# Optimization experiments

Hardware: AMD Instinct MI355X
Metric: run time of the kernel (lower is better)

## Reference

```python
import jax, jax.numpy as jnp
import numpy as np


def setup_inputs() -> dict:
    key = jax.random.key(0)
    k1, k2, k3 = jax.random.split(key, 3)
    H, W, C = 200, 200, 512
    NUM_ROIS = 300
    img = jax.random.normal(k1, (1, H, W, C), dtype=jnp.float32)
    # rois[0, r] = (x, y, w, h); ensure crops are in-bounds and non-empty
    xy = jax.random.randint(k2, (1, NUM_ROIS, 2), 0, 100)
    wh = jax.random.randint(k3, (1, NUM_ROIS, 2), 1, 100)
    rois = jnp.concatenate([xy, wh], axis=-1).astype(jnp.int32)
    return {"img": img, "rois": rois, "pool_size": 7}


def reference(img, rois, pool_size):
    """RoiPoolingConv: per-ROI crop + legacy-TF bilinear resize, vectorized.

    img:  [1, H, W, C] float feature map
    rois: [1, R, 4] int (x, y, w, h) in feature-map pixels
    returns [1, R, P, P, C]
    """
    P = pool_size
    img0 = img[0]                              # [H, W, C]
    H, W, C = img0.shape
    x = rois[0, :, 0].astype(jnp.int32)        # [R]
    y = rois[0, :, 1].astype(jnp.int32)
    w = rois[0, :, 2].astype(jnp.int32)
    h = rois[0, :, 3].astype(jnp.int32)

    out_idx = jnp.arange(P, dtype=jnp.float32)  # [P]
    # legacy tf.image.resize_images (bilinear, align_corners=False):
    #   src = out_idx * (in_size / out_size); corners floor(src), floor(src)+1 clipped
    sy = y[:, None].astype(jnp.float32) + out_idx[None, :] * (h[:, None].astype(jnp.float32) / P)  # [R,P]
    sx = x[:, None].astype(jnp.float32) + out_idx[None, :] * (w[:, None].astype(jnp.float32) / P)  # [R,P]

    y0 = jnp.floor(sy).astype(jnp.int32)
    x0 = jnp.floor(sx).astype(jnp.int32)
    y1 = jnp.minimum(y0 + 1, y[:, None] + h[:, None] - 1)  # clip to crop bottom edge
    x1 = jnp.minimum(x0 + 1, x[:, None] + w[:, None] - 1)
    # safety clamp to image bounds
    y0 = jnp.clip(y0, 0, H - 1); y1 = jnp.clip(y1, 0, H - 1)
    x0 = jnp.clip(x0, 0, W - 1); x1 = jnp.clip(x1, 0, W - 1)

    wy = (sy - jnp.floor(sy))[:, :, None, None]  # [R,P,1,1]
    wx = (sx - jnp.floor(sx))[:, None, :, None]  # [R,1,P,1]

    # gather the 4 corners for all ROIs at once -> [R,P,P,C]
    v00 = img0[y0[:, :, None], x0[:, None, :]]
    v01 = img0[y0[:, :, None], x1[:, None, :]]
    v10 = img0[y1[:, :, None], x0[:, None, :]]
    v11 = img0[y1[:, :, None], x1[:, None, :]]

    top = v00 * (1.0 - wx) + v01 * wx
    bot = v10 * (1.0 - wx) + v11 * wx
    out = top * (1.0 - wy) + bot * wy          # [R,P,P,C]
    return out[None]                           # [1,R,P,P,C]
```

## Files before the change

kernel.cpp:

```cpp
#include <hip/hip_runtime.h>
#include <hip/hip_bf16.h>
#include <cmath>


__global__ __launch_bounds__(448) void roi_pool_kernel(
    const float* __restrict__ img, const int* __restrict__ rois,
    float* __restrict__ out, int P, int H, int W, int C) {
  const int b = blockIdx.x;
  const int r = b / P;
  const int i = b - r * P;
  const int j = threadIdx.x >> 6;
  const int lane = threadIdx.x & 63;

  const int x = rois[r * 4 + 0];
  const int y = rois[r * 4 + 1];
  const int w = rois[r * 4 + 2];
  const int h = rois[r * 4 + 3];

  const float Pf = (float)P;
  const float sy = (float)y + (float)i * ((float)h / Pf);
  const float sx = (float)x + (float)j * ((float)w / Pf);
  const float fy = floorf(sy);
  const float fx = floorf(sx);
  int y0 = (int)fy;
  int x0 = (int)fx;
  int y1 = min(y0 + 1, y + h - 1);
  int x1 = min(x0 + 1, x + w - 1);
  y0 = min(max(y0, 0), H - 1);
  y1 = min(max(y1, 0), H - 1);
  x0 = min(max(x0, 0), W - 1);
  x1 = min(max(x1, 0), W - 1);
  const float wy = sy - fy;
  const float wx = sx - fx;
  const float omwx = 1.0f - wx;
  const float omwy = 1.0f - wy;

  const float* __restrict__ p00 = img + ((size_t)y0 * W + x0) * C;
  const float* __restrict__ p01 = img + ((size_t)y0 * W + x1) * C;
  const float* __restrict__ p10 = img + ((size_t)y1 * W + x0) * C;
  const float* __restrict__ p11 = img + ((size_t)y1 * W + x1) * C;
  float* __restrict__ po = out + ((size_t)b * P + j) * C;

  for (int c = lane * 8; c < C; c += 64 * 8) {
    const float4 a00 = *reinterpret_cast<const float4*>(p00 + c);
    const float4 b00 = *reinterpret_cast<const float4*>(p00 + c + 4);
    const float4 a01 = *reinterpret_cast<const float4*>(p01 + c);
    const float4 b01 = *reinterpret_cast<const float4*>(p01 + c + 4);
    const float4 a10 = *reinterpret_cast<const float4*>(p10 + c);
    const float4 b10 = *reinterpret_cast<const float4*>(p10 + c + 4);
    const float4 a11 = *reinterpret_cast<const float4*>(p11 + c);
    const float4 b11 = *reinterpret_cast<const float4*>(p11 + c + 4);

    float4 oa, ob;
#define LERP1(F, v00_, v01_, v10_, v11_)                      \
    {                                                          \
      const float top = v00_.F * omwx + v01_.F * wx;           \
      const float bot = v10_.F * omwx + v11_.F * wx;           \
      oa.F = top * omwy + bot * wy;                            \
    }
#define LERP2(F, v00_, v01_, v10_, v11_)                      \
    {                                                          \
      const float top = v00_.F * omwx + v01_.F * wx;           \
      const float bot = v10_.F * omwx + v11_.F * wx;           \
      ob.F = top * omwy + bot * wy;                            \
    }
    LERP1(x, a00, a01, a10, a11)
    LERP1(y, a00, a01, a10, a11)
    LERP1(z, a00, a01, a10, a11)
    LERP1(w, a00, a01, a10, a11)
    LERP2(x, b00, b01, b10, b11)
    LERP2(y, b00, b01, b10, b11)
    LERP2(z, b00, b01, b10, b11)
    LERP2(w, b00, b01, b10, b11)
#undef LERP1
#undef LERP2
    *reinterpret_cast<float4*>(po + c) = oa;
    *reinterpret_cast<float4*>(po + c + 4) = ob;
  }
}

extern "C" void kernel_launch(void* const* d_in, const int* in_sizes, int n_in,
                              void* d_out, int out_size, void* d_ws, size_t ws_size,
                              hipStream_t stream) {
  const float* img = (const float*)d_in[0];
  const int* rois = (const int*)d_in[1];
  float* out = (float*)d_out;

  const int H = 200, W = 200, C = 512;
  const int R = in_sizes[1] / 4;
  const int pp = out_size / (R * C);
  int P = 1;
  while ((P + 1) * (P + 1) <= pp) ++P;

  const int blocks = R * P;
  roi_pool_kernel<<<blocks, P * 64, 0, stream>>>(img, rois, out, P, H, W, C);
}
```

Measured before the change: 24.89 us.

## Sort ROI rows by source y and map contiguous ranges to XCDs for L2 locality

Adds a single-block counting-sort kernel that orders (roi,row) work items by their source row, and remaps block IDs so each XCD processes a contiguous range of sorted items. The goal is for blocks sharing an XCD L2 to read overlapping image rows and so reuse cached data instead of fetching from HBM. The cost is an extra serial kernel launch plus a dependent perm lookup before the main kernel can start.

```diff
diff --git a/kernel.cpp b/kernel.cpp
--- a/kernel.cpp
+++ b/kernel.cpp
@@ -3,12 +3,71 @@
 #include <cmath>
 
 
+__global__ __launch_bounds__(256) void roi_sort_kernel(
+    const int* __restrict__ rois, int* __restrict__ perm, int R, int P, int H) {
+  __shared__ int bins[256];
+  __shared__ int offs[256];
+  const int tid = threadIdx.x;
+  bins[tid] = 0;
+  __syncthreads();
+  const int N = R * P;
+  const float Pf = (float)P;
+  for (int idx = tid; idx < N; idx += 256) {
+    const int r = idx / P;
+    const int i = idx - r * P;
+    const int y = rois[r * 4 + 1];
+    const int h = rois[r * 4 + 3];
+    const float sy = (float)y + (float)i * ((float)h / Pf);
+    int key = (int)floorf(sy);
+    key = min(max(key, 0), 255);
+    atomicAdd(&bins[key], 1);
+  }
+  __syncthreads();
+  if (tid < 64) {
+    int s0 = 0;
+#pragma unroll
+    for (int k = 0; k < 4; ++k) s0 += bins[tid * 4 + k];
+    int ex = s0;
+#pragma unroll
+    for (int d = 1; d < 64; d <<= 1) {
+      int t = __shfl_up(ex, d);
+      if ((tid & 63) >= d) ex += t;
+    }
+    ex -= s0;
+    int acc = ex;
+#pragma unroll
+    for (int k = 0; k < 4; ++k) {
+      offs[tid * 4 + k] = acc;
+      acc += bins[tid * 4 + k];
+    }
+  }
+  __syncthreads();
+  for (int idx = tid; idx < N; idx += 256) {
+    const int r = idx / P;
+    const int i = idx - r * P;
+    const int y = rois[r * 4 + 1];
+    const int h = rois[r * 4 + 3];
+    const float sy = (float)y + (float)i * ((float)h / Pf);
+    int key = (int)floorf(sy);
+    key = min(max(key, 0), 255);
+    const int pos = atomicAdd(&offs[key], 1);
+    perm[pos] = idx;
+  }
+}
+
 __global__ __launch_bounds__(448) void roi_pool_kernel(
     const float* __restrict__ img, const int* __restrict__ rois,
-    float* __restrict__ out, int P, int H, int W, int C) {
-  const int b = blockIdx.x;
-  const int r = b / P;
-  const int i = b - r * P;
+    const int* __restrict__ perm,
+    float* __restrict__ out, int P, int H, int W, int C, int nblk) {
+  const int q = nblk >> 3;
+  const int rr = nblk & 7;
+  const int xcd = blockIdx.x & 7;
+  const int base = (xcd < rr) ? xcd * (q + 1) : rr * (q + 1) + (xcd - rr) * q;
+  const int s = base + (blockIdx.x >> 3);
+
+  const int item = perm[s];
+  const int r = item / P;
+  const int i = item - r * P;
   const int j = threadIdx.x >> 6;
   const int lane = threadIdx.x & 63;
 
@@ -39,7 +98,7 @@
   const float* __restrict__ p01 = img + ((size_t)y0 * W + x1) * C;
   const float* __restrict__ p10 = img + ((size_t)y1 * W + x0) * C;
   const float* __restrict__ p11 = img + ((size_t)y1 * W + x1) * C;
-  float* __restrict__ po = out + ((size_t)b * P + j) * C;
+  float* __restrict__ po = out + ((size_t)item * P + j) * C;
 
   for (int c = lane * 8; c < C; c += 64 * 8) {
     const float4 a00 = *reinterpret_cast<const float4*>(p00 + c);
@@ -52,28 +111,21 @@
     const float4 b11 = *reinterpret_cast<const float4*>(p11 + c + 4);
 
     float4 oa, ob;
-#define LERP1(F, v00_, v01_, v10_, v11_)                      \
+#define LERP(DST, F, v00_, v01_, v10_, v11_)                  \
     {                                                          \
       const float top = v00_.F * omwx + v01_.F * wx;           \
       const float bot = v10_.F * omwx + v11_.F * wx;           \
-      oa.F = top * omwy + bot * wy;                            \
+      DST.F = top * omwy + bot * wy;                           \
     }
-#define LERP2(F, v00_, v01_, v10_, v11_)                      \
-    {                                                          \
-      const float top = v00_.F * omwx + v01_.F * wx;           \
-      const float bot = v10_.F * omwx + v11_.F * wx;           \
-      ob.F = top * omwy + bot * wy;                            \
-    }
-    LERP1(x, a00, a01, a10, a11)
-    LERP1(y, a00, a01, a10, a11)
-    LERP1(z, a00, a01, a10, a11)
-    LERP1(w, a00, a01, a10, a11)
-    LERP2(x, b00, b01, b10, b11)
-    LERP2(y, b00, b01, b10, b11)
-    LERP2(z, b00, b01, b10, b11)
-    LERP2(w, b00, b01, b10, b11)
-#undef LERP1
-#undef LERP2
+    LERP(oa, x, a00, a01, a10, a11)
+    LERP(oa, y, a00, a01, a10, a11)
+    LERP(oa, z, a00, a01, a10, a11)
+    LERP(oa, w, a00, a01, a10, a11)
+    LERP(ob, x, b00, b01, b10, b11)
+    LERP(ob, y, b00, b01, b10, b11)
+    LERP(ob, z, b00, b01, b10, b11)
+    LERP(ob, w, b00, b01, b10, b11)
+#undef LERP
     *reinterpret_cast<float4*>(po + c) = oa;
     *reinterpret_cast<float4*>(po + c + 4) = ob;
   }
@@ -85,6 +137,7 @@
   const float* img = (const float*)d_in[0];
   const int* rois = (const int*)d_in[1];
   float* out = (float*)d_out;
+  int* perm = (int*)d_ws;
 
   const int H = 200, W = 200, C = 512;
   const int R = in_sizes[1] / 4;
@@ -92,6 +145,7 @@
   int P = 1;
   while ((P + 1) * (P + 1) <= pp) ++P;
 
-  const int blocks = R * P;
-  roi_pool_kernel<<<blocks, P * 64, 0, stream>>>(img, rois, out, P, H, W, C);
+  const int nblk = R * P;
+  roi_sort_kernel<<<1, 256, 0, stream>>>(rois, perm, R, P, H);
+  roi_pool_kernel<<<nblk, P * 64, 0, stream>>>(img, rois, perm, out, P, H, W, C, nblk);
 }
```

After: 26.62 us. 1.07x slower.
